# Optimization experiments

Measured on AMD Instinct MI355X. Metric: run time of the kernel, lower is better.

The kernel has to match this reference:

```python
import jax, jax.numpy as jnp
import numpy as np

B, S, D, H, L, V = 4, 512, 1024, 16, 4, 32000
DH = D // H
LATENT_START, N_LATENT, LATENT_ID = 64, 6, 5


def _ln(x, g, b):
    m = x.mean(-1, keepdims=True)
    v = ((x - m) ** 2).mean(-1, keepdims=True)
    return (x - m) * jax.lax.rsqrt(v + 1e-5) * g + b


def _model(x_emb, pos_ids, pos_emb, Wqkv, Wo, W1, W2, ln1_g, ln1_b, ln2_g, ln2_b, lnf_g, lnf_b, lm_head):
    # x_emb: [B,T,D]; returns (last_hidden [B,T,D] after final LN, logits [B,T,V])
    b, T, _ = x_emb.shape
    x = x_emb + pos_emb[pos_ids]
    causal = jnp.tril(jnp.ones((T, T), bool))
    for l in range(L):
        h = _ln(x, ln1_g[l], ln1_b[l])
        q, k, v = jnp.split(h @ Wqkv[l], 3, axis=-1)
        q = q.reshape(b, T, H, DH).transpose(0, 2, 1, 3)
        k = k.reshape(b, T, H, DH).transpose(0, 2, 1, 3)
        v = v.reshape(b, T, H, DH).transpose(0, 2, 1, 3)
        scores = jnp.einsum('bhqd,bhkd->bhqk', q, k) / np.float32(np.sqrt(DH))
        scores = jnp.where(causal, scores, jnp.float32(-1e9))
        attn = jax.nn.softmax(scores, axis=-1)
        o = jnp.einsum('bhqk,bhkd->bhqd', attn, v).transpose(0, 2, 1, 3).reshape(b, T, D)
        x = x + o @ Wo[l]
        h2 = _ln(x, ln2_g[l], ln2_b[l])
        x = x + jax.nn.gelu(h2 @ W1[l]) @ W2[l]
    hid = _ln(x, lnf_g, lnf_b)  # GPT2 hidden_states[-1] is post ln_f
    return hid, hid @ lm_head


def setup_inputs() -> dict:
    key = jax.random.key(0)
    ks = jax.random.split(key, 10)
    input_ids = jax.random.randint(ks[0], (B, S), 0, V, dtype=jnp.int32)
    input_ids = input_ids.at[:, LATENT_START:LATENT_START + N_LATENT].set(LATENT_ID)
    attention_mask = jnp.ones((B, S), jnp.int32)
    labels = jax.random.randint(ks[1], (B, S), 0, V, dtype=jnp.int32)
    position_ids = jnp.broadcast_to(jnp.arange(S, dtype=jnp.int32), (B, S))
    s = 0.02
    return {
        'input_ids': input_ids, 'attention_mask': attention_mask,
        'labels': labels, 'position_ids': position_ids,
        'emb': jax.random.normal(ks[2], (V, D), jnp.float32) * s,
        'pos_emb': jax.random.normal(ks[3], (S, D), jnp.float32) * s,
        'Wqkv': jax.random.normal(ks[4], (L, D, 3 * D), jnp.float32) * s,
        'Wo': jax.random.normal(ks[5], (L, D, D), jnp.float32) * s,
        'W1': jax.random.normal(ks[6], (L, D, 4 * D), jnp.float32) * s,
        'W2': jax.random.normal(ks[7], (L, 4 * D, D), jnp.float32) * s,
        'ln1_g': jnp.ones((L, D), jnp.float32), 'ln1_b': jnp.zeros((L, D), jnp.float32),
        'ln2_g': jnp.ones((L, D), jnp.float32), 'ln2_b': jnp.zeros((L, D), jnp.float32),
        'lnf_g': jnp.ones((D,), jnp.float32), 'lnf_b': jnp.zeros((D,), jnp.float32),
        'lm_head': jax.random.normal(ks[8], (D, V), jnp.float32) * s,
    }


def reference(input_ids, attention_mask, labels, position_ids, emb, pos_emb, Wqkv, Wo, W1, W2, ln1_g, ln1_b, ln2_g, ln2_b, lnf_g, lnf_b, lm_head):
    params = (pos_emb, Wqkv, Wo, W1, W2, ln1_g, ln1_b, ln2_g, ln2_b, lnf_g, lnf_b, lm_head)
    inputs_embeds = emb[input_ids]  # [B,S,D]
    start, end = 0, LATENT_START
    logits_list = []
    for p in range(N_LATENT):  # iterative latent passes
        hid, lg = _model(inputs_embeds[:, :end], position_ids[:, :end], *params)
        logits_list.append(lg[:, start:end])
        pos = LATENT_START + p
        # vectorized scatter: splice previous-position hidden state into latent slot
        inputs_embeds = inputs_embeds.at[:, pos, :].set(hid[:, pos - 1, :])
        start, end = end, (S if p + 1 >= N_LATENT else end + 1)
    hid, lg = _model(inputs_embeds[:, :end], position_ids[:, :end], *params)
    logits_list.append(lg[:, start:end])
    logits = jnp.concatenate(logits_list, axis=1)  # [B,S,V]
    shift_logits = logits[:, :-1]
    shift_labels = labels[:, 1:]
    logp = jax.nn.log_softmax(shift_logits, axis=-1)
    loss = -jnp.take_along_axis(logp, shift_labels[..., None], axis=-1).mean()
    return loss, inputs_embeds, logits
```

## Files before the change

kernel.cpp:

```cpp
#include <hip/hip_runtime.h>

static constexpr int BB  = 4;
static constexpr int SS  = 512;
static constexpr int DD  = 1024;
static constexpr int HH  = 16;
static constexpr int LL  = 4;
static constexpr int VV  = 32000;
static constexpr int DHH = 64;
static constexpr int FFF = 4096;

typedef short bf16x8  __attribute__((ext_vector_type(8)));
typedef short bf16x4v __attribute__((ext_vector_type(4)));
typedef float f32x4   __attribute__((ext_vector_type(4)));

__device__ __forceinline__ float b2f(ushort u){
  union { float f; unsigned int u32; } x; x.u32 = ((unsigned int)u) << 16; return x.f;
}
__device__ __forceinline__ ushort f2b(float f){
  union { float f; unsigned int u32; } x; x.f = f;
  unsigned int u = x.u32;
  return (ushort)((u + 0x7FFFu + ((u >> 16) & 1u)) >> 16);
}

__global__ __launch_bounds__(256) void convT_k(const float* __restrict__ in, ushort* __restrict__ out,
                                               int K, int N, long inStride, long outStride)
{
  in  += (long)blockIdx.z * inStride;
  out += (long)blockIdx.z * outStride;
  __shared__ float tile[64][65];
  int n0 = blockIdx.x * 64, k0 = blockIdx.y * 64;
  int tid = threadIdx.x;
  int cc = tid & 63, rr = tid >> 6;
#pragma unroll
  for (int i = 0; i < 16; i++){
    int r = rr + i * 4;
    tile[r][cc] = in[(long)(k0 + r) * N + n0 + cc];
  }
  __syncthreads();
#pragma unroll
  for (int i = 0; i < 16; i++){
    int r = rr + i * 4;
    out[(long)(n0 + r) * K + k0 + cc] = f2b(tile[cc][r]);
  }
}

__global__ __launch_bounds__(256) void embed_k(const int* __restrict__ ids, const float* __restrict__ emb,
                                               const float* __restrict__ pe, float* __restrict__ x,
                                               float* __restrict__ oemb)
{
  int t = blockIdx.x, b = blockIdx.y, tid = threadIdx.x;
  int id = ids[b * SS + t];
  float4 ev = *((const float4*)(emb + (long)id * DD) + tid);
  float4 pv = *((const float4*)(pe  + (long)t  * DD) + tid);
  *((float4*)(x + (long)(t * BB + b) * DD) + tid) =
      make_float4(ev.x + pv.x, ev.y + pv.y, ev.z + pv.z, ev.w + pv.w);
  float* op = oemb + ((long)b * SS + t) * DD + tid * 4;
  op[0] = ev.x; op[1] = ev.y; op[2] = ev.z; op[3] = ev.w;
}

__global__ __launch_bounds__(256) void ln_k(const float* __restrict__ xin, const float* __restrict__ g,
                                            const float* __restrict__ bt, ushort* __restrict__ out, long row0)
{
  long row = row0 + blockIdx.x;
  int tid = threadIdx.x;
  const float* rp = xin + row * DD;
  float4 v = *(const float4*)(rp + tid * 4);
  float s1 = v.x + v.y + v.z + v.w;
  float s2 = v.x * v.x + v.y * v.y + v.z * v.z + v.w * v.w;
#pragma unroll
  for (int o = 32; o; o >>= 1){ s1 += __shfl_down(s1, o); s2 += __shfl_down(s2, o); }
  __shared__ float red[2][4];
  int wv = tid >> 6, lane = tid & 63;
  if (lane == 0){ red[0][wv] = s1; red[1][wv] = s2; }
  __syncthreads();
  s1 = red[0][0] + red[0][1] + red[0][2] + red[0][3];
  s2 = red[1][0] + red[1][1] + red[1][2] + red[1][3];
  float mean = s1 * (1.0f / DD);
  float var  = s2 * (1.0f / DD) - mean * mean;
  float rstd = rsqrtf(var + 1e-5f);
  float4 gv = *(const float4*)(g + tid * 4);
  float4 bv = *(const float4*)(bt + tid * 4);
  ushort4 o4;
  o4.x = f2b((v.x - mean) * rstd * gv.x + bv.x);
  o4.y = f2b((v.y - mean) * rstd * gv.y + bv.y);
  o4.z = f2b((v.z - mean) * rstd * gv.z + bv.z);
  o4.w = f2b((v.w - mean) * rstd * gv.w + bv.w);
  *(ushort4*)(out + row * DD + tid * 4) = o4;
}

template<int EPI>
__device__ __forceinline__ void epi_store(float v, int grow, int ocol, void* Cv, int ldc,
                                          const float* Add, int t0, int l,
                                          ushort* kc, ushort* vc, ushort* qb)
{
  if constexpr (EPI == 1){
    float* Cf = (float*)Cv; long idx = (long)grow * ldc + ocol;
    Cf[idx] = v + Add[idx];
  } else if constexpr (EPI == 2){
    ushort* Cb = (ushort*)Cv; long idx = (long)grow * ldc + ocol;
    float tt = 0.7978845608028654f * (v + 0.044715f * v * v * v);
    Cb[idx] = f2b(0.5f * v * (1.0f + tanhf(tt)));
  } else if constexpr (EPI == 3){
    int t = t0 + (grow >> 2), b = grow & 3;
    ((float*)Cv)[((long)b * SS + t) * VV + ocol] = v;
  } else if constexpr (EPI == 4){
    if (ocol < DD){
      qb[((long)(t0 * BB + grow)) * DD + ocol] = f2b(v);
    } else {
      int t = t0 + (grow >> 2), b = grow & 3;
      int h = (ocol >> 6) & 15, d = ocol & 63;
      long dst = (((long)l * BB + b) * HH + h) * ((long)SS * DHH) + (long)t * DHH + d;
      if (ocol >= 2 * DD) vc[dst] = f2b(v); else kc[dst] = f2b(v);
    }
  }
}

template<int EPI>
__global__ __launch_bounds__(256) void gemm_k(const ushort* __restrict__ A, int lda,
                                              const ushort* __restrict__ BT,
                                              void* Cv, int ldc,
                                              const float* Add,
                                              int M, int N, int K, int gx,
                                              int l, int t0,
                                              ushort* kc, ushort* vc, ushort* qb,
                                              float* part, int KS)
{
  constexpr int BM  = 128;
  constexpr int MFR = 4;
  constexpr int NFR = 4;
  __shared__ ushort As[BM][72];
  __shared__ ushort Bs[128][72];
  int tid = threadIdx.x;
  int wv = tid >> 6, lane = tid & 63;
  int wm = wv >> 1, wn = wv & 1;

  int nwg = gridDim.x, orig = blockIdx.x;
  int wgid;
  if (nwg <= 1024){
    int qq = nwg >> 3, rr8 = nwg & 7, xcd = orig & 7;
    wgid = ((xcd < rr8) ? xcd * (qq + 1) : rr8 * (qq + 1) + (xcd - rr8) * qq) + (orig >> 3);
  } else {
    wgid = orig;
  }

  int gxy = gx * (N >> 7);
  int ksId = wgid / gxy;
  int rem  = wgid - ksId * gxy;
  int bx = rem % gx, by = rem / gx;
  int m0 = bx * BM, n0 = by * 128;
  int Kc = K / KS;
  int k_beg = ksId * Kc, k_end = k_beg + Kc;

  f32x4 acc[MFR][NFR];
  f32x4 zz = {0.f, 0.f, 0.f, 0.f};
#pragma unroll
  for (int m = 0; m < MFR; m++)
#pragma unroll
    for (int n = 0; n < NFR; n++) acc[m][n] = zz;

  int g4 = (lane >> 4) * 4;
  int rA = lane & 15;
  int arow = tid >> 3;
  int acol = (tid & 7) * 8;

  const ushort* Bp = BT + (long)(n0 + arow) * K + acol;
  long sB = 32 * (long)K;
  int gr0 = m0 + arow;       if (gr0 > M - 1) gr0 = M - 1;
  int gr1 = m0 + 32 + arow;  if (gr1 > M - 1) gr1 = M - 1;
  int gr2 = m0 + 64 + arow;  if (gr2 > M - 1) gr2 = M - 1;
  int gr3 = m0 + 96 + arow;  if (gr3 > M - 1) gr3 = M - 1;
  const ushort* Ap0 = A + (long)gr0 * lda + acol;
  const ushort* Ap1 = A + (long)gr1 * lda + acol;
  const ushort* Ap2 = A + (long)gr2 * lda + acol;
  const ushort* Ap3 = A + (long)gr3 * lda + acol;

  uint4 b0 = *(const uint4*)(Bp + k_beg);
  uint4 b1 = *(const uint4*)(Bp + sB + k_beg);
  uint4 b2 = *(const uint4*)(Bp + 2 * sB + k_beg);
  uint4 b3 = *(const uint4*)(Bp + 3 * sB + k_beg);
  uint4 a0 = *(const uint4*)(Ap0 + k_beg);
  uint4 a1 = *(const uint4*)(Ap1 + k_beg);
  uint4 a2 = *(const uint4*)(Ap2 + k_beg);
  uint4 a3 = *(const uint4*)(Ap3 + k_beg);

  for (int k0 = k_beg; k0 < k_end; k0 += 64){
    *(uint4*)&Bs[arow     ][acol] = b0;
    *(uint4*)&Bs[arow + 32][acol] = b1;
    *(uint4*)&Bs[arow + 64][acol] = b2;
    *(uint4*)&Bs[arow + 96][acol] = b3;
    *(uint4*)&As[arow     ][acol] = a0;
    *(uint4*)&As[arow + 32][acol] = a1;
    *(uint4*)&As[arow + 64][acol] = a2;
    *(uint4*)&As[arow + 96][acol] = a3;
    __syncthreads();
    int kn = k0 + 64;
    if (kn < k_end){
      b0 = *(const uint4*)(Bp + kn);
      b1 = *(const uint4*)(Bp + sB + kn);
      b2 = *(const uint4*)(Bp + 2 * sB + kn);
      b3 = *(const uint4*)(Bp + 3 * sB + kn);
      a0 = *(const uint4*)(Ap0 + kn);
      a1 = *(const uint4*)(Ap1 + kn);
      a2 = *(const uint4*)(Ap2 + kn);
      a3 = *(const uint4*)(Ap3 + kn);
    }
#pragma unroll
    for (int kk = 0; kk < 64; kk += 32){
      bf16x8 af[MFR], bfr[NFR];
#pragma unroll
      for (int m = 0; m < MFR; m++){
        int row = wm * 64 + m * 16 + rA;
        bf16x4v lo = *(const bf16x4v*)&As[row][kk + g4];
        bf16x4v hi = *(const bf16x4v*)&As[row][kk + 16 + g4];
        af[m] = __builtin_shufflevector(lo, hi, 0, 1, 2, 3, 4, 5, 6, 7);
      }
#pragma unroll
      for (int n = 0; n < NFR; n++){
        int row = wn * 64 + n * 16 + rA;
        bf16x4v lo = *(const bf16x4v*)&Bs[row][kk + g4];
        bf16x4v hi = *(const bf16x4v*)&Bs[row][kk + 16 + g4];
        bfr[n] = __builtin_shufflevector(lo, hi, 0, 1, 2, 3, 4, 5, 6, 7);
      }
#pragma unroll
      for (int m = 0; m < MFR; m++)
#pragma unroll
        for (int n = 0; n < NFR; n++)
          acc[m][n] = __builtin_amdgcn_mfma_f32_16x16x32_bf16(af[m], bfr[n], acc[m][n], 0, 0, 0);
    }
    __syncthreads();
  }

  int r4 = (lane >> 4) * 4;
#pragma unroll
  for (int m = 0; m < MFR; m++){
#pragma unroll
    for (int n = 0; n < NFR; n++){
      int orow = wm * 64 + m * 16 + r4;
      int ocol = n0 + wn * 64 + n * 16 + rA;
#pragma unroll
      for (int r = 0; r < 4; r++){
        int grow = m0 + orow + r;
        if (grow < M){
          if (KS > 1)
            part[(long)ksId * M * N + (long)grow * N + ocol] = acc[m][n][r];
          else
            epi_store<EPI>(acc[m][n][r], grow, ocol, Cv, ldc, Add, t0, l, kc, vc, qb);
        }
      }
    }
  }
}

template<int EPI>
__global__ __launch_bounds__(256) void sred_k(const float* __restrict__ part, int KS, int M, int N,
                                              void* Cv, int ldc, const float* Add,
                                              int l, int t0, ushort* kc, ushort* vc, ushort* qb)
{
  long i = (long)blockIdx.x * 256 + threadIdx.x;
  long MN = (long)M * N;
  if (i >= MN) return;
  float v = 0.f;
  for (int s = 0; s < KS; s++) v += part[s * MN + i];
  int m = (int)(i / N), n = (int)(i - (long)m * N);
  epi_store<EPI>(v, m, n, Cv, ldc, Add, t0, l, kc, vc, qb);
}

template<int TYPE>
__global__ __launch_bounds__(256) void dec_gemv_k(const float* xf, const ushort* ab,
                                                  const float* g, const float* bt,
                                                  const ushort* WT, float* x,
                                                  ushort* qb, ushort* kc, ushort* vc, ushort* gb,
                                                  int l, int pos)
{
  constexpr int K   = (TYPE == 3) ? FFF : DD;
  constexpr int NCH = K / 1024;
  int tid = threadIdx.x, wid = tid >> 6, lane = tid & 63;
  int n = blockIdx.x * 4 + wid;

  float acc[4] = {0.f, 0.f, 0.f, 0.f};

#pragma unroll
  for (int ch = 0; ch < NCH; ch++){
    int ks = ch * 1024 + lane * 16;
    float a[4][16];
    if constexpr (TYPE == 0 || TYPE == 2){
#pragma unroll
      for (int r = 0; r < 4; r++){
        const float* rp = xf + (long)(pos * BB + r) * DD + ks;
#pragma unroll
        for (int q = 0; q < 4; q++){
          float4 v = *(const float4*)(rp + q * 4);
          a[r][q*4+0] = v.x; a[r][q*4+1] = v.y; a[r][q*4+2] = v.z; a[r][q*4+3] = v.w;
        }
      }
      float gj[16], bj[16];
#pragma unroll
      for (int q = 0; q < 4; q++){
        float4 gv = *(const float4*)(g  + ks + q * 4);
        float4 bv = *(const float4*)(bt + ks + q * 4);
        gj[q*4+0]=gv.x; gj[q*4+1]=gv.y; gj[q*4+2]=gv.z; gj[q*4+3]=gv.w;
        bj[q*4+0]=bv.x; bj[q*4+1]=bv.y; bj[q*4+2]=bv.z; bj[q*4+3]=bv.w;
      }
#pragma unroll
      for (int r = 0; r < 4; r++){
        float s1 = 0.f, s2 = 0.f;
#pragma unroll
        for (int j = 0; j < 16; j++){ s1 += a[r][j]; s2 += a[r][j] * a[r][j]; }
#pragma unroll
        for (int o = 32; o; o >>= 1){ s1 += __shfl_xor(s1, o); s2 += __shfl_xor(s2, o); }
        float mean = s1 * (1.0f / DD);
        float var  = s2 * (1.0f / DD) - mean * mean;
        float rstd = rsqrtf(var + 1e-5f);
#pragma unroll
        for (int j = 0; j < 16; j++)
          a[r][j] = b2f(f2b((a[r][j] - mean) * rstd * gj[j] + bj[j]));
      }
    } else {
      constexpr int AD = (TYPE == 3) ? FFF : DD;
#pragma unroll
      for (int r = 0; r < 4; r++){
        const ushort* rp = ab + (long)(pos * BB + r) * AD + ks;
        uint4 pa = *(const uint4*)rp;
        uint4 pb = *(const uint4*)(rp + 8);
        const unsigned int w[8] = {pa.x, pa.y, pa.z, pa.w, pb.x, pb.y, pb.z, pb.w};
#pragma unroll
        for (int q = 0; q < 8; q++){
          a[r][q*2]   = b2f((ushort)(w[q] & 0xffff));
          a[r][q*2+1] = b2f((ushort)(w[q] >> 16));
        }
      }
    }
    {
      const ushort* wp = WT + (long)n * K + ks;
      uint4 pa = *(const uint4*)wp;
      uint4 pb = *(const uint4*)(wp + 8);
      const unsigned int w[8] = {pa.x, pa.y, pa.z, pa.w, pb.x, pb.y, pb.z, pb.w};
      float wf[16];
#pragma unroll
      for (int q = 0; q < 8; q++){
        wf[q*2]   = b2f((ushort)(w[q] & 0xffff));
        wf[q*2+1] = b2f((ushort)(w[q] >> 16));
      }
#pragma unroll
      for (int r = 0; r < 4; r++){
        float s = 0.f;
#pragma unroll
        for (int j = 0; j < 16; j++) s += a[r][j] * wf[j];
        acc[r] += s;
      }
    }
  }

#pragma unroll
  for (int r = 0; r < 4; r++)
#pragma unroll
    for (int o = 32; o; o >>= 1) acc[r] += __shfl_xor(acc[r], o);

  if (lane < 4){
    int r = lane;
    long Rrow = (long)(pos * BB + r);
    float v = acc[r];
    if constexpr (TYPE == 0){
      if (n < DD){
        qb[Rrow * DD + n] = f2b(v);
      } else if (n < 2 * DD){
        int h = (n - DD) >> 6, d = n & 63;
        kc[(((long)l * BB + r) * HH + h) * ((long)SS * DHH) + (long)pos * DHH + d] = f2b(v);
      } else {
        int h = (n - 2 * DD) >> 6, d = n & 63;
        vc[(((long)l * BB + r) * HH + h) * ((long)SS * DHH) + (long)pos * DHH + d] = f2b(v);
      }
    } else if constexpr (TYPE == 2){
      float tt = 0.7978845608028654f * (v + 0.044715f * v * v * v);
      gb[Rrow * FFF + n] = f2b(0.5f * v * (1.0f + tanhf(tt)));
    } else {
      long idx = Rrow * DD + n;
      x[idx] = x[idx] + v;
    }
  }
}

__global__ __launch_bounds__(256) void dec_final_k(const float* xf, const float* g, const float* bt,
                                                   const float* pe, ushort* hid, float* x,
                                                   float* oemb, int pos)
{
  int wid = threadIdx.x >> 6, lane = threadIdx.x & 63;
  long R = (long)(pos * BB + wid);
  const float* rp = xf + R * DD + lane * 16;
  float a[16];
#pragma unroll
  for (int q = 0; q < 4; q++){
    float4 v = *(const float4*)(rp + q * 4);
    a[q*4+0] = v.x; a[q*4+1] = v.y; a[q*4+2] = v.z; a[q*4+3] = v.w;
  }
  float s1 = 0.f, s2 = 0.f;
#pragma unroll
  for (int j = 0; j < 16; j++){ s1 += a[j]; s2 += a[j] * a[j]; }
#pragma unroll
  for (int o = 32; o; o >>= 1){ s1 += __shfl_xor(s1, o); s2 += __shfl_xor(s2, o); }
  float mean = s1 * (1.0f / DD);
  float var  = s2 * (1.0f / DD) - mean * mean;
  float rstd = rsqrtf(var + 1e-5f);
  int pn = pos + 1;
#pragma unroll
  for (int j = 0; j < 16; j++){
    int d = lane * 16 + j;
    ushort hb = f2b((a[j] - mean) * rstd * g[d] + bt[d]);
    hid[R * DD + d] = hb;
    float hv = b2f(hb);
    oemb[((long)wid * SS + pn) * DD + d] = hv;
    x[((long)(pn * BB + wid)) * DD + d] = hv + pe[(long)pn * DD + d];
  }
}

__global__ __launch_bounds__(256) void attn_k(const ushort* __restrict__ qb, const ushort* __restrict__ kc,
                                              const ushort* __restrict__ vc, ushort* __restrict__ o,
                                              int l, int t0, int Tc)
{
  __shared__ float sc[4][512];
  __shared__ float qs[4][64];
  int tid = threadIdx.x, wv = tid >> 6, lane = tid & 63;
  int b = blockIdx.z, h = blockIdx.y;
  int qrow = blockIdx.x * 4 + wv;
  bool act = qrow < Tc;
  int tq = t0 + qrow;
  long kvoff = (((long)l * BB + b) * HH + h) * ((long)SS * DHH);
  const ushort* kb = kc + kvoff;
  const ushort* vb = vc + kvoff;
  if (act) qs[wv][lane] = b2f(qb[((long)(tq * BB + b)) * DD + h * DHH + lane]);
  __syncthreads();
  int nk = act ? (tq + 1) : 0;
  float m = -3.0e38f;
  for (int key = lane; key < nk; key += 64){
    const ushort* kp = kb + (long)key * DHH;
    float s = 0.f;
#pragma unroll
    for (int j = 0; j < 8; j++){
      uint4 kvv = *(const uint4*)(kp + j * 8);
      s += qs[wv][j*8+0] * b2f((ushort)(kvv.x & 0xffff));
      s += qs[wv][j*8+1] * b2f((ushort)(kvv.x >> 16));
      s += qs[wv][j*8+2] * b2f((ushort)(kvv.y & 0xffff));
      s += qs[wv][j*8+3] * b2f((ushort)(kvv.y >> 16));
      s += qs[wv][j*8+4] * b2f((ushort)(kvv.z & 0xffff));
      s += qs[wv][j*8+5] * b2f((ushort)(kvv.z >> 16));
      s += qs[wv][j*8+6] * b2f((ushort)(kvv.w & 0xffff));
      s += qs[wv][j*8+7] * b2f((ushort)(kvv.w >> 16));
    }
    s *= 0.125f;
    sc[wv][key] = s;
    m = fmaxf(m, s);
  }
#pragma unroll
  for (int off = 32; off; off >>= 1) m = fmaxf(m, __shfl_xor(m, off));
  float ssum = 0.f;
  for (int key = lane; key < nk; key += 64){
    float p = expf(sc[wv][key] - m);
    sc[wv][key] = p;
    ssum += p;
  }
#pragma unroll
  for (int off = 32; off; off >>= 1) ssum += __shfl_xor(ssum, off);
  __syncthreads();
  float accv = 0.f;
  int key = 0;
  for (; key + 3 < nk; key += 4){
    float p0 = sc[wv][key],     p1 = sc[wv][key + 1];
    float p2 = sc[wv][key + 2], p3 = sc[wv][key + 3];
    float v0 = b2f(vb[(long)key * DHH + lane]);
    float v1 = b2f(vb[(long)(key + 1) * DHH + lane]);
    float v2 = b2f(vb[(long)(key + 2) * DHH + lane]);
    float v3 = b2f(vb[(long)(key + 3) * DHH + lane]);
    accv += p0 * v0 + p1 * v1 + p2 * v2 + p3 * v3;
  }
  for (; key < nk; key++)
    accv += sc[wv][key] * b2f(vb[(long)key * DHH + lane]);
  if (act) o[((long)(tq * BB + b)) * DD + h * DHH + lane] = f2b(accv / ssum);
}

__global__ __launch_bounds__(256) void advance_k(const ushort* __restrict__ hid, const float* __restrict__ pe,
                                                 float* __restrict__ x, float* __restrict__ oemb, int pos)
{
  int d = blockIdx.x * 256 + threadIdx.x;
  int b = blockIdx.y;
  float hv = b2f(hid[((long)((pos - 1) * BB + b)) * DD + d]);
  oemb[((long)b * SS + pos) * DD + d] = hv;
  x[((long)(pos * BB + b)) * DD + d] = hv + pe[(long)pos * DD + d];
}

__global__ __launch_bounds__(256) void loss_rows_k(const float* __restrict__ logits, const int* __restrict__ labels,
                                                   float* __restrict__ rowloss)
{
  int t = blockIdx.x, b = blockIdx.y, tid = threadIdx.x;
  const float* row = logits + ((long)b * SS + t) * VV;
  float m = -3.0e38f, s = 0.f;
  auto upd = [&](float v){
    if (v > m){ s = s * expf(m - v) + 1.f; m = v; }
    else s += expf(v - m);
  };
  if (tid < 3) upd(row[tid]);
  if (tid == 3) upd(row[VV - 1]);
  const float4* vrow = (const float4*)(row + 3);
  for (int i = tid; i < 7999; i += 256){
    float4 v = vrow[i];
    upd(v.x); upd(v.y); upd(v.z); upd(v.w);
  }
#pragma unroll
  for (int off = 32; off; off >>= 1){
    float om = __shfl_xor(m, off), os = __shfl_xor(s, off);
    float nm = fmaxf(m, om);
    s = s * expf(m - nm) + os * expf(om - nm);
    m = nm;
  }
  __shared__ float sm[4], ssb[4];
  if ((tid & 63) == 0){ sm[tid >> 6] = m; ssb[tid >> 6] = s; }
  __syncthreads();
  if (tid == 0){
    float M = fmaxf(fmaxf(sm[0], sm[1]), fmaxf(sm[2], sm[3]));
    float S = ssb[0] * expf(sm[0] - M) + ssb[1] * expf(sm[1] - M)
            + ssb[2] * expf(sm[2] - M) + ssb[3] * expf(sm[3] - M);
    int lab = labels[b * SS + t + 1];
    rowloss[b * (SS - 1) + t] = (M + logf(S)) - row[lab];
  }
}

__global__ __launch_bounds__(256) void loss_final_k(const float* __restrict__ rowloss, float* __restrict__ out)
{
  int tid = threadIdx.x;
  float s = 0.f;
  for (int i = tid; i < BB * (SS - 1); i += 256) s += rowloss[i];
#pragma unroll
  for (int o = 32; o; o >>= 1) s += __shfl_down(s, o);
  __shared__ float red[4];
  if ((tid & 63) == 0) red[tid >> 6] = s;
  __syncthreads();
  if (tid == 0) out[0] = (red[0] + red[1] + red[2] + red[3]) / (float)(BB * (SS - 1));
}

static inline int cdiv_i(int a, int b){ return (a + b - 1) / b; }

extern "C" void kernel_launch(void* const* d_in, const int* in_sizes, int n_in,
                              void* d_out, int out_size, void* d_ws, size_t ws_size,
                              hipStream_t stream)
{
  (void)in_sizes; (void)n_in; (void)out_size; (void)ws_size;
  const int*   ids    = (const int*)d_in[0];
  const int*   labels = (const int*)d_in[2];
  const float* emb    = (const float*)d_in[4];
  const float* pe     = (const float*)d_in[5];
  const float* Wqkv   = (const float*)d_in[6];
  const float* Wo     = (const float*)d_in[7];
  const float* W1     = (const float*)d_in[8];
  const float* W2     = (const float*)d_in[9];
  const float* ln1g   = (const float*)d_in[10];
  const float* ln1b   = (const float*)d_in[11];
  const float* ln2g   = (const float*)d_in[12];
  const float* ln2b   = (const float*)d_in[13];
  const float* lnfg   = (const float*)d_in[14];
  const float* lnfb   = (const float*)d_in[15];
  const float* lm     = (const float*)d_in[16];

  float* out_loss   = (float*)d_out;
  float* out_emb    = out_loss + 1;
  float* out_logits = out_emb + (size_t)BB * SS * DD;

  char* wsp = (char*)d_ws;
  size_t off = 0;
  auto alloc = [&](size_t bytes) -> void* {
    void* p = wsp + off; off += (bytes + 255) & ~(size_t)255; return p;
  };
  ushort* wqkvT = (ushort*)alloc((size_t)LL * 3 * DD * DD * 2);
  ushort* woT   = (ushort*)alloc((size_t)LL * DD * DD * 2);
  ushort* w1T   = (ushort*)alloc((size_t)LL * FFF * DD * 2);
  ushort* w2T   = (ushort*)alloc((size_t)LL * DD * FFF * 2);
  ushort* lmT   = (ushort*)alloc((size_t)VV * DD * 2);
  float*  x     = (float*)alloc((size_t)BB * SS * DD * 4);
  ushort* hbuf  = (ushort*)alloc((size_t)BB * SS * DD * 2);
  ushort* qbuf  = (ushort*)alloc((size_t)BB * SS * DD * 2);
  ushort* obuf  = (ushort*)alloc((size_t)BB * SS * DD * 2);
  ushort* gbuf  = (ushort*)alloc((size_t)BB * SS * FFF * 2);
  ushort* hid   = (ushort*)alloc((size_t)BB * SS * DD * 2);
  ushort* kcache= (ushort*)alloc((size_t)LL * BB * SS * DD * 2);
  ushort* vcache= (ushort*)alloc((size_t)LL * BB * SS * DD * 2);
  float*  rowls = (float*)alloc((size_t)BB * (SS - 1) * 4);
  float*  part  = out_logits;

  convT_k<<<dim3(3 * DD / 64, DD / 64, LL), dim3(256), 0, stream>>>(Wqkv, wqkvT, DD, 3 * DD, (long)DD * 3 * DD, (long)3 * DD * DD);
  convT_k<<<dim3(DD / 64, DD / 64, LL),     dim3(256), 0, stream>>>(Wo,   woT,  DD, DD,     (long)DD * DD,     (long)DD * DD);
  convT_k<<<dim3(FFF / 64, DD / 64, LL),    dim3(256), 0, stream>>>(W1,   w1T,  DD, FFF,    (long)DD * FFF,    (long)FFF * DD);
  convT_k<<<dim3(DD / 64, FFF / 64, LL),    dim3(256), 0, stream>>>(W2,   w2T,  FFF, DD,    (long)FFF * DD,    (long)DD * FFF);
  convT_k<<<dim3(VV / 64, DD / 64, 1),      dim3(256), 0, stream>>>(lm,   lmT,  DD, VV,     0, 0);

  embed_k<<<dim3(SS, BB), dim3(256), 0, stream>>>(ids, emb, pe, x, out_emb);

  const int ct0[7] = {0, 64, 65, 66, 67, 68, 69};
  const int ct1[7] = {64, 65, 66, 67, 68, 69, 512};

  auto g128 = [&](int epi, const ushort* A, int lda, const ushort* BT, void* C, int ldc,
                  const float* Add, int M, int N, int K, int l, int t0, int KS){
    int gx = cdiv_i(M, 128);
    int nwg = gx * (N >> 7) * KS;
    if (epi == 1) gemm_k<1><<<nwg, 256, 0, stream>>>(A, lda, BT, C, ldc, Add, M, N, K, gx, l, t0, kcache, vcache, qbuf, part, KS);
    if (epi == 2) gemm_k<2><<<nwg, 256, 0, stream>>>(A, lda, BT, C, ldc, Add, M, N, K, gx, l, t0, kcache, vcache, qbuf, part, KS);
    if (epi == 3) gemm_k<3><<<nwg, 256, 0, stream>>>(A, lda, BT, C, ldc, Add, M, N, K, gx, l, t0, kcache, vcache, qbuf, part, KS);
    if (epi == 4) gemm_k<4><<<nwg, 256, 0, stream>>>(A, lda, BT, C, ldc, Add, M, N, K, gx, l, t0, kcache, vcache, qbuf, part, KS);
    if (KS > 1){
      int nred = cdiv_i(M * N, 256);
      if (epi == 1) sred_k<1><<<nred, 256, 0, stream>>>(part, KS, M, N, C, ldc, Add, l, t0, kcache, vcache, qbuf);
      if (epi == 2) sred_k<2><<<nred, 256, 0, stream>>>(part, KS, M, N, C, ldc, Add, l, t0, kcache, vcache, qbuf);
      if (epi == 4) sred_k<4><<<nred, 256, 0, stream>>>(part, KS, M, N, C, ldc, Add, l, t0, kcache, vcache, qbuf);
    }
  };

  for (int c = 0; c < 7; c++){
    int t0 = ct0[c];
    int Tc = ct1[c] - t0;
    int M  = Tc * BB;
    long roff = (long)t0 * BB;

    if (Tc == 1){
      int pos = t0;
      for (int l = 0; l < LL; l++){
        dec_gemv_k<0><<<dim3(3 * DD / 4), dim3(256), 0, stream>>>(x, nullptr, ln1g + l * DD, ln1b + l * DD,
            wqkvT + (long)l * 3 * DD * DD, nullptr, qbuf, kcache, vcache, nullptr, l, pos);
        attn_k<<<dim3(1, HH, BB), dim3(64), 0, stream>>>(qbuf, kcache, vcache, obuf, l, t0, Tc);
        dec_gemv_k<1><<<dim3(DD / 4), dim3(256), 0, stream>>>(nullptr, obuf, nullptr, nullptr,
            woT + (long)l * DD * DD, x, nullptr, nullptr, nullptr, nullptr, l, pos);
        dec_gemv_k<2><<<dim3(FFF / 4), dim3(256), 0, stream>>>(x, nullptr, ln2g + l * DD, ln2b + l * DD,
            w1T + (long)l * FFF * DD, nullptr, nullptr, nullptr, nullptr, gbuf, l, pos);
        dec_gemv_k<3><<<dim3(DD / 4), dim3(256), 0, stream>>>(nullptr, gbuf, nullptr, nullptr,
            w2T + (long)l * DD * FFF, x, nullptr, nullptr, nullptr, nullptr, l, pos);
      }
      dec_final_k<<<dim3(1), dim3(256), 0, stream>>>(x, lnfg, lnfb, pe, hid, x, out_emb, pos);
    } else {
      bool small = (M <= 256);
      int ksQKV = small ? 4 : 2;
      int ksWO  = small ? 8 : 2;
      int ksW1  = small ? 4 : 2;
      int ksW2  = small ? 8 : 2;
      for (int l = 0; l < LL; l++){
        ln_k<<<dim3(M), dim3(256), 0, stream>>>(x, ln1g + l * DD, ln1b + l * DD, hbuf, roff);
        g128(4, hbuf + roff * DD, DD, wqkvT + (long)l * 3 * DD * DD, nullptr, 0, nullptr, M, 3 * DD, DD, l, t0, ksQKV);
        attn_k<<<dim3(cdiv_i(Tc, 4), HH, BB), dim3(256), 0, stream>>>(qbuf, kcache, vcache, obuf, l, t0, Tc);
        g128(1, obuf + roff * DD, DD, woT + (long)l * DD * DD, x + roff * DD, DD, x + roff * DD, M, DD, DD, l, t0, ksWO);
        ln_k<<<dim3(M), dim3(256), 0, stream>>>(x, ln2g + l * DD, ln2b + l * DD, hbuf, roff);
        g128(2, hbuf + roff * DD, DD, w1T + (long)l * FFF * DD, gbuf + roff * FFF, FFF, nullptr, M, FFF, DD, l, t0, ksW1);
        g128(1, gbuf + roff * FFF, FFF, w2T + (long)l * DD * FFF, x + roff * DD, DD, x + roff * DD, M, DD, FFF, l, t0, ksW2);
      }
      ln_k<<<dim3(M), dim3(256), 0, stream>>>(x, lnfg, lnfb, hid, roff);
      if (c == 0)
        advance_k<<<dim3(DD / 256, BB), dim3(256), 0, stream>>>(hid, pe, x, out_emb, 64);
    }
  }

  g128(3, hid, DD, lmT, out_logits, 0, nullptr, BB * SS, VV, DD, 0, 0, 1);

  loss_rows_k<<<dim3(SS - 1, BB), dim3(256), 0, stream>>>(out_logits, labels, rowls);
  loss_final_k<<<dim3(1), dim3(256), 0, stream>>>(rowls, out_loss);
}
```

Measured before the change: 2.934 ms.

## Add 128x256-tile GEMM for LM head and drop split-K for large QKV/W1

Adds a new 512-thread MFMA GEMM kernel with 128x256 tiles and register-prefetched global loads, used for the large LM-head projection in place of the generic 128-tile GEMM. Its epilogue writes logits directly in [B,S,V] order. Separately, split-K is turned off for the QKV and W1 GEMMs when M is large, which removes the partial-sum buffer round trip and the reduction kernel. The larger tile uses more LDS and registers, so occupancy may drop, and the single-split GEMMs launch fewer workgroups.

```diff
diff --git a/kernel.cpp b/kernel.cpp
--- a/kernel.cpp
+++ b/kernel.cpp
@@ -251,6 +251,111 @@
   }
 }
 
+__global__ __launch_bounds__(512) void gemm256_k(const ushort* __restrict__ A, int lda,
+                                                 const ushort* __restrict__ BT,
+                                                 float* __restrict__ Cv,
+                                                 int M, int N, int K, int gx, int t0)
+{
+  constexpr int MFR = 4;
+  constexpr int NFR = 4;
+  __shared__ ushort As[128][72];
+  __shared__ ushort Bs[256][72];
+  int tid = threadIdx.x;
+  int wv = tid >> 6, lane = tid & 63;
+  int wm = wv >> 2, wn = wv & 3;
+
+  int wgid = blockIdx.x;
+  int bx = wgid % gx, by = wgid / gx;
+  int m0 = bx * 128, n0 = by * 256;
+
+  f32x4 acc[MFR][NFR];
+  f32x4 zz = {0.f, 0.f, 0.f, 0.f};
+#pragma unroll
+  for (int m = 0; m < MFR; m++)
+#pragma unroll
+    for (int n = 0; n < NFR; n++) acc[m][n] = zz;
+
+  int g4 = (lane >> 4) * 4;
+  int rA = lane & 15;
+  int srow = tid >> 3;
+  int scol = (tid & 7) * 8;
+
+  long sB = 64 * (long)K;
+  const ushort* Bp = BT + (long)(n0 + srow) * K + scol;
+  int ga0 = m0 + srow;       if (ga0 > M - 1) ga0 = M - 1;
+  int ga1 = m0 + 64 + srow;  if (ga1 > M - 1) ga1 = M - 1;
+  const ushort* Ap0 = A + (long)ga0 * lda + scol;
+  const ushort* Ap1 = A + (long)ga1 * lda + scol;
+
+  uint4 b0 = *(const uint4*)(Bp);
+  uint4 b1 = *(const uint4*)(Bp + sB);
+  uint4 b2 = *(const uint4*)(Bp + 2 * sB);
+  uint4 b3 = *(const uint4*)(Bp + 3 * sB);
+  uint4 a0 = *(const uint4*)(Ap0);
+  uint4 a1 = *(const uint4*)(Ap1);
+
+  for (int k0 = 0; k0 < K; k0 += 64){
+    *(uint4*)&Bs[srow      ][scol] = b0;
+    *(uint4*)&Bs[srow + 64 ][scol] = b1;
+    *(uint4*)&Bs[srow + 128][scol] = b2;
+    *(uint4*)&Bs[srow + 192][scol] = b3;
+    *(uint4*)&As[srow      ][scol] = a0;
+    *(uint4*)&As[srow + 64 ][scol] = a1;
+    __syncthreads();
+    int kn = k0 + 64;
+    if (kn < K){
+      b0 = *(const uint4*)(Bp + kn);
+      b1 = *(const uint4*)(Bp + sB + kn);
+      b2 = *(const uint4*)(Bp + 2 * sB + kn);
+      b3 = *(const uint4*)(Bp + 3 * sB + kn);
+      a0 = *(const uint4*)(Ap0 + kn);
+      a1 = *(const uint4*)(Ap1 + kn);
+    }
+#pragma unroll
+    for (int kk = 0; kk < 64; kk += 32){
+      bf16x8 af[MFR], bfr[NFR];
+#pragma unroll
+      for (int m = 0; m < MFR; m++){
+        int row = wm * 64 + m * 16 + rA;
+        bf16x4v lo = *(const bf16x4v*)&As[row][kk + g4];
+        bf16x4v hi = *(const bf16x4v*)&As[row][kk + 16 + g4];
+        af[m] = __builtin_shufflevector(lo, hi, 0, 1, 2, 3, 4, 5, 6, 7);
+      }
+#pragma unroll
+      for (int n = 0; n < NFR; n++){
+        int row = wn * 64 + n * 16 + rA;
+        bf16x4v lo = *(const bf16x4v*)&Bs[row][kk + g4];
+        bf16x4v hi = *(const bf16x4v*)&Bs[row][kk + 16 + g4];
+        bfr[n] = __builtin_shufflevector(lo, hi, 0, 1, 2, 3, 4, 5, 6, 7);
+      }
+#pragma unroll
+      for (int m = 0; m < MFR; m++)
+#pragma unroll
+        for (int n = 0; n < NFR; n++)
+          acc[m][n] = __builtin_amdgcn_mfma_f32_16x16x32_bf16(af[m], bfr[n], acc[m][n], 0, 0, 0);
+    }
+    __syncthreads();
+  }
+
+  int r4 = (lane >> 4) * 4;
+#pragma unroll
+  for (int m = 0; m < MFR; m++){
+#pragma unroll
+    for (int n = 0; n < NFR; n++){
+      int orow = wm * 64 + m * 16 + r4;
+      int ocol = n0 + wn * 64 + n * 16 + rA;
+#pragma unroll
+      for (int r = 0; r < 4; r++){
+        int grow = m0 + orow + r;
+        if (grow < M){
+          int t = t0 + (grow >> 2), b = grow & 3;
+          Cv[((long)b * SS + t) * VV + ocol] = acc[m][n][r];
+        }
+      }
+    }
+  }
+}
+
 template<int EPI>
 __global__ __launch_bounds__(256) void sred_k(const float* __restrict__ part, int KS, int M, int N,
                                               void* Cv, int ldc, const float* Add,
@@ -633,9 +738,9 @@
       dec_final_k<<<dim3(1), dim3(256), 0, stream>>>(x, lnfg, lnfb, pe, hid, x, out_emb, pos);
     } else {
       bool small = (M <= 256);
-      int ksQKV = small ? 4 : 2;
+      int ksQKV = small ? 4 : 1;
       int ksWO  = small ? 8 : 2;
-      int ksW1  = small ? 4 : 2;
+      int ksW1  = small ? 4 : 1;
       int ksW2  = small ? 8 : 2;
       for (int l = 0; l < LL; l++){
         ln_k<<<dim3(M), dim3(256), 0, stream>>>(x, ln1g + l * DD, ln1b + l * DD, hbuf, roff);
@@ -652,7 +757,11 @@
     }
   }
 
-  g128(3, hid, DD, lmT, out_logits, 0, nullptr, BB * SS, VV, DD, 0, 0, 1);
+  {
+    int gx = BB * SS / 128;
+    int nwg = gx * (VV / 256);
+    gemm256_k<<<nwg, 512, 0, stream>>>(hid, DD, lmT, out_logits, BB * SS, VV, DD, gx, 0);
+  }
 
   loss_rows_k<<<dim3(SS - 1, BB), dim3(256), 0, stream>>>(out_logits, labels, rowls);
   loss_final_k<<<dim3(1), dim3(256), 0, stream>>>(rowls, out_loss);
```

Result: no change. 2.879 ms (-1.9%).

## Fuse decode steps into a persistent cooperative kernel with grid syncs

Applied to the files above, without the earlier changes.

Replaces the roughly 105 small per-layer decode kernel launches for the five single-token latent steps with one persistent cooperative kernel. It uses grid-wide syncs between the QKV, attention, Wo, W1 and W2 phases and the final LN. It also moves the split-K partial buffer into its own workspace allocation instead of aliasing the logits, and lowers split-K for the large chunk's QKV and W1 GEMMs from 2 to 1. The aim is to remove launch overhead and tail idle time; the cost is 25 grid barriers per step on only 256 blocks, which may underuse bandwidth for the weight streaming.

```diff
diff --git a/kernel.cpp b/kernel.cpp
--- a/kernel.cpp
+++ b/kernel.cpp
@@ -1,4 +1,5 @@
 #include <hip/hip_runtime.h>
+#include <hip/hip_cooperative_groups.h>
 
 static constexpr int BB  = 4;
 static constexpr int SS  = 512;
@@ -413,6 +414,248 @@
   }
 }
 
+struct DecParams {
+  const float* pe;
+  float* x;
+  ushort* qb; ushort* kc; ushort* vc; ushort* gb; ushort* ob;
+  ushort* hid; float* oemb;
+  const ushort* wqkvT; const ushort* woT; const ushort* w1T; const ushort* w2T;
+  const float* ln1g; const float* ln1b; const float* ln2g; const float* ln2b;
+  const float* lnfg; const float* lnfb;
+};
+
+template<int TYPE>
+__device__ __forceinline__ void dec_gemv_ln_phase(const DecParams& p, int l, int pos,
+                                                  int gw, int nw, int lane)
+{
+  constexpr int NCOLS = (TYPE == 0) ? 3 * DD : FFF;
+  const ushort* WT = (TYPE == 0) ? p.wqkvT + (long)l * 3 * DD * DD
+                                 : p.w1T   + (long)l * FFF * DD;
+  const float* g  = ((TYPE == 0) ? p.ln1g : p.ln2g) + l * DD;
+  const float* bt = ((TYPE == 0) ? p.ln1b : p.ln2b) + l * DD;
+  int ks = lane * 16;
+  float a[4][16];
+#pragma unroll
+  for (int r = 0; r < 4; r++){
+    const float* rp = p.x + (long)(pos * BB + r) * DD + ks;
+#pragma unroll
+    for (int q = 0; q < 4; q++){
+      float4 v = *(const float4*)(rp + q * 4);
+      a[r][q*4+0] = v.x; a[r][q*4+1] = v.y; a[r][q*4+2] = v.z; a[r][q*4+3] = v.w;
+    }
+  }
+  float gj[16], bj[16];
+#pragma unroll
+  for (int q = 0; q < 4; q++){
+    float4 gv = *(const float4*)(g  + ks + q * 4);
+    float4 bv = *(const float4*)(bt + ks + q * 4);
+    gj[q*4+0]=gv.x; gj[q*4+1]=gv.y; gj[q*4+2]=gv.z; gj[q*4+3]=gv.w;
+    bj[q*4+0]=bv.x; bj[q*4+1]=bv.y; bj[q*4+2]=bv.z; bj[q*4+3]=bv.w;
+  }
+#pragma unroll
+  for (int r = 0; r < 4; r++){
+    float s1 = 0.f, s2 = 0.f;
+#pragma unroll
+    for (int j = 0; j < 16; j++){ s1 += a[r][j]; s2 += a[r][j] * a[r][j]; }
+#pragma unroll
+    for (int o = 32; o; o >>= 1){ s1 += __shfl_xor(s1, o); s2 += __shfl_xor(s2, o); }
+    float mean = s1 * (1.0f / DD);
+    float var  = s2 * (1.0f / DD) - mean * mean;
+    float rstd = rsqrtf(var + 1e-5f);
+#pragma unroll
+    for (int j = 0; j < 16; j++)
+      a[r][j] = b2f(f2b((a[r][j] - mean) * rstd * gj[j] + bj[j]));
+  }
+  for (int n = gw; n < NCOLS; n += nw){
+    const ushort* wp = WT + (long)n * DD + ks;
+    uint4 pa = *(const uint4*)wp;
+    uint4 pb = *(const uint4*)(wp + 8);
+    const unsigned int w[8] = {pa.x, pa.y, pa.z, pa.w, pb.x, pb.y, pb.z, pb.w};
+    float wf[16];
+#pragma unroll
+    for (int q = 0; q < 8; q++){
+      wf[q*2]   = b2f((ushort)(w[q] & 0xffff));
+      wf[q*2+1] = b2f((ushort)(w[q] >> 16));
+    }
+    float acc[4];
+#pragma unroll
+    for (int r = 0; r < 4; r++){
+      float s = 0.f;
+#pragma unroll
+      for (int j = 0; j < 16; j++) s += a[r][j] * wf[j];
+      acc[r] = s;
+    }
+#pragma unroll
+    for (int r = 0; r < 4; r++)
+#pragma unroll
+      for (int o = 32; o; o >>= 1) acc[r] += __shfl_xor(acc[r], o);
+    if (lane < 4){
+      int r = lane;
+      long Rrow = (long)(pos * BB + r);
+      float v = acc[r];
+      if constexpr (TYPE == 0){
+        if (n < DD){
+          p.qb[Rrow * DD + n] = f2b(v);
+        } else if (n < 2 * DD){
+          int h = (n - DD) >> 6, d = n & 63;
+          p.kc[(((long)l * BB + r) * HH + h) * ((long)SS * DHH) + (long)pos * DHH + d] = f2b(v);
+        } else {
+          int h = (n - 2 * DD) >> 6, d = n & 63;
+          p.vc[(((long)l * BB + r) * HH + h) * ((long)SS * DHH) + (long)pos * DHH + d] = f2b(v);
+        }
+      } else {
+        float tt = 0.7978845608028654f * (v + 0.044715f * v * v * v);
+        p.gb[Rrow * FFF + n] = f2b(0.5f * v * (1.0f + tanhf(tt)));
+      }
+    }
+  }
+}
+
+template<int TYPE>
+__device__ __forceinline__ void dec_gemv_res_phase(const DecParams& p, int l, int pos,
+                                                   int gw, int nw, int lane)
+{
+  constexpr int K   = (TYPE == 3) ? FFF : DD;
+  constexpr int NCH = K / 1024;
+  const ushort* WT = (TYPE == 1) ? p.woT + (long)l * DD * DD : p.w2T + (long)l * DD * FFF;
+  const ushort* ab = (TYPE == 1) ? p.ob : p.gb;
+  for (int n = gw; n < DD; n += nw){
+    float acc[4] = {0.f, 0.f, 0.f, 0.f};
+#pragma unroll
+    for (int ch = 0; ch < NCH; ch++){
+      int ks = ch * 1024 + lane * 16;
+      const ushort* wp = WT + (long)n * K + ks;
+      uint4 wa = *(const uint4*)wp;
+      uint4 wb = *(const uint4*)(wp + 8);
+      const unsigned int w[8] = {wa.x, wa.y, wa.z, wa.w, wb.x, wb.y, wb.z, wb.w};
+      float wf[16];
+#pragma unroll
+      for (int q = 0; q < 8; q++){
+        wf[q*2]   = b2f((ushort)(w[q] & 0xffff));
+        wf[q*2+1] = b2f((ushort)(w[q] >> 16));
+      }
+#pragma unroll
+      for (int r = 0; r < 4; r++){
+        const ushort* rp = ab + (long)(pos * BB + r) * K + ks;
+        uint4 xa = *(const uint4*)rp;
+        uint4 xb = *(const uint4*)(rp + 8);
+        const unsigned int xw[8] = {xa.x, xa.y, xa.z, xa.w, xb.x, xb.y, xb.z, xb.w};
+        float s = 0.f;
+#pragma unroll
+        for (int q = 0; q < 8; q++){
+          s += b2f((ushort)(xw[q] & 0xffff)) * wf[q*2];
+          s += b2f((ushort)(xw[q] >> 16))    * wf[q*2+1];
+        }
+        acc[r] += s;
+      }
+    }
+#pragma unroll
+    for (int r = 0; r < 4; r++)
+#pragma unroll
+      for (int o = 32; o; o >>= 1) acc[r] += __shfl_xor(acc[r], o);
+    if (lane < 4){
+      long idx = (long)(pos * BB + lane) * DD + n;
+      p.x[idx] = p.x[idx] + acc[lane];
+    }
+  }
+}
+
+__global__ __launch_bounds__(256) void dec_all_k(DecParams p)
+{
+  cooperative_groups::grid_group grid = cooperative_groups::this_grid();
+  int tid = threadIdx.x, wid = tid >> 6, lane = tid & 63;
+  int gw = blockIdx.x * 4 + wid;
+  int nw = gridDim.x * 4;
+  __shared__ float qs[4][64];
+  __shared__ float ps[4][80];
+
+  for (int step = 0; step < 5; step++){
+    int pos = 64 + step;
+    for (int l = 0; l < LL; l++){
+      dec_gemv_ln_phase<0>(p, l, pos, gw, nw, lane);
+      __threadfence(); grid.sync(); __threadfence();
+      if (gw < BB * HH){
+        int b = gw >> 4, h = gw & 15;
+        long kvoff = (((long)l * BB + b) * HH + h) * ((long)SS * DHH);
+        const ushort* kb = p.kc + kvoff;
+        const ushort* vb = p.vc + kvoff;
+        qs[wid][lane] = b2f(p.qb[((long)(pos * BB + b)) * DD + h * DHH + lane]);
+        int nk = pos + 1;
+        float m = -3.0e38f;
+        for (int key = lane; key < nk; key += 64){
+          const ushort* kp = kb + (long)key * DHH;
+          float s = 0.f;
+#pragma unroll
+          for (int j = 0; j < 8; j++){
+            uint4 kvv = *(const uint4*)(kp + j * 8);
+            s += qs[wid][j*8+0] * b2f((ushort)(kvv.x & 0xffff));
+            s += qs[wid][j*8+1] * b2f((ushort)(kvv.x >> 16));
+            s += qs[wid][j*8+2] * b2f((ushort)(kvv.y & 0xffff));
+            s += qs[wid][j*8+3] * b2f((ushort)(kvv.y >> 16));
+            s += qs[wid][j*8+4] * b2f((ushort)(kvv.z & 0xffff));
+            s += qs[wid][j*8+5] * b2f((ushort)(kvv.z >> 16));
+            s += qs[wid][j*8+6] * b2f((ushort)(kvv.w & 0xffff));
+            s += qs[wid][j*8+7] * b2f((ushort)(kvv.w >> 16));
+          }
+          s *= 0.125f;
+          ps[wid][key] = s;
+          m = fmaxf(m, s);
+        }
+#pragma unroll
+        for (int off = 32; off; off >>= 1) m = fmaxf(m, __shfl_xor(m, off));
+        float ssum = 0.f;
+        for (int key = lane; key < nk; key += 64){
+          float pv = expf(ps[wid][key] - m);
+          ps[wid][key] = pv;
+          ssum += pv;
+        }
+#pragma unroll
+        for (int off = 32; off; off >>= 1) ssum += __shfl_xor(ssum, off);
+        float accv = 0.f;
+        for (int key = 0; key < nk; key++)
+          accv += ps[wid][key] * b2f(vb[(long)key * DHH + lane]);
+        p.ob[((long)(pos * BB + b)) * DD + h * DHH + lane] = f2b(accv / ssum);
+      }
+      __threadfence(); grid.sync(); __threadfence();
+      dec_gemv_res_phase<1>(p, l, pos, gw, nw, lane);
+      __threadfence(); grid.sync(); __threadfence();
+      dec_gemv_ln_phase<2>(p, l, pos, gw, nw, lane);
+      __threadfence(); grid.sync(); __threadfence();
+      dec_gemv_res_phase<3>(p, l, pos, gw, nw, lane);
+      __threadfence(); grid.sync(); __threadfence();
+    }
+    if (blockIdx.x == 0){
+      long R = (long)(pos * BB + wid);
+      const float* rp = p.x + R * DD + lane * 16;
+      float a[16];
+#pragma unroll
+      for (int q = 0; q < 4; q++){
+        float4 v = *(const float4*)(rp + q * 4);
+        a[q*4+0] = v.x; a[q*4+1] = v.y; a[q*4+2] = v.z; a[q*4+3] = v.w;
+      }
+      float s1 = 0.f, s2 = 0.f;
+#pragma unroll
+      for (int j = 0; j < 16; j++){ s1 += a[j]; s2 += a[j] * a[j]; }
+#pragma unroll
+      for (int o = 32; o; o >>= 1){ s1 += __shfl_xor(s1, o); s2 += __shfl_xor(s2, o); }
+      float mean = s1 * (1.0f / DD);
+      float var  = s2 * (1.0f / DD) - mean * mean;
+      float rstd = rsqrtf(var + 1e-5f);
+      int pn = pos + 1;
+#pragma unroll
+      for (int j = 0; j < 16; j++){
+        int d = lane * 16 + j;
+        ushort hb = f2b((a[j] - mean) * rstd * p.lnfg[d] + p.lnfb[d]);
+        p.hid[R * DD + d] = hb;
+        float hv = b2f(hb);
+        p.oemb[((long)wid * SS + pn) * DD + d] = hv;
+        p.x[((long)(pn * BB + wid)) * DD + d] = hv + p.pe[(long)pn * DD + d];
+      }
+    }
+    __threadfence(); grid.sync(); __threadfence();
+  }
+}
+
 __global__ __launch_bounds__(256) void attn_k(const ushort* __restrict__ qb, const ushort* __restrict__ kc,
                                               const ushort* __restrict__ vc, ushort* __restrict__ o,
                                               int l, int t0, int Tc)
@@ -581,8 +824,8 @@
   ushort* hid   = (ushort*)alloc((size_t)BB * SS * DD * 2);
   ushort* kcache= (ushort*)alloc((size_t)LL * BB * SS * DD * 2);
   ushort* vcache= (ushort*)alloc((size_t)LL * BB * SS * DD * 2);
+  float*  part  = (float*)alloc((size_t)17 * 1024 * 1024);
   float*  rowls = (float*)alloc((size_t)BB * (SS - 1) * 4);
-  float*  part  = out_logits;
 
   convT_k<<<dim3(3 * DD / 64, DD / 64, LL), dim3(256), 0, stream>>>(Wqkv, wqkvT, DD, 3 * DD, (long)DD * 3 * DD, (long)3 * DD * DD);
   convT_k<<<dim3(DD / 64, DD / 64, LL),     dim3(256), 0, stream>>>(Wo,   woT,  DD, DD,     (long)DD * DD,     (long)DD * DD);
@@ -591,9 +834,6 @@
   convT_k<<<dim3(VV / 64, DD / 64, 1),      dim3(256), 0, stream>>>(lm,   lmT,  DD, VV,     0, 0);
 
   embed_k<<<dim3(SS, BB), dim3(256), 0, stream>>>(ids, emb, pe, x, out_emb);
-
-  const int ct0[7] = {0, 64, 65, 66, 67, 68, 69};
-  const int ct1[7] = {64, 65, 66, 67, 68, 69, 512};
 
   auto g128 = [&](int epi, const ushort* A, int lda, const ushort* BT, void* C, int ldc,
                   const float* Add, int M, int N, int K, int l, int t0, int KS){
@@ -611,18 +851,45 @@
     }
   };
 
-  for (int c = 0; c < 7; c++){
-    int t0 = ct0[c];
-    int Tc = ct1[c] - t0;
-    int M  = Tc * BB;
+  auto big_chunk = [&](int t0, int Tc){
+    int M = Tc * BB;
     long roff = (long)t0 * BB;
-
-    if (Tc == 1){
-      int pos = t0;
+    bool small = (M <= 256);
+    int ksQKV = small ? 4 : 1;
+    int ksWO  = small ? 8 : 2;
+    int ksW1  = small ? 4 : 1;
+    int ksW2  = small ? 8 : 2;
+    for (int l = 0; l < LL; l++){
+      ln_k<<<dim3(M), dim3(256), 0, stream>>>(x, ln1g + l * DD, ln1b + l * DD, hbuf, roff);
+      g128(4, hbuf + roff * DD, DD, wqkvT + (long)l * 3 * DD * DD, nullptr, 0, nullptr, M, 3 * DD, DD, l, t0, ksQKV);
+      attn_k<<<dim3(cdiv_i(Tc, 4), HH, BB), dim3(256), 0, stream>>>(qbuf, kcache, vcache, obuf, l, t0, Tc);
+      g128(1, obuf + roff * DD, DD, woT + (long)l * DD * DD, x + roff * DD, DD, x + roff * DD, M, DD, DD, l, t0, ksWO);
+      ln_k<<<dim3(M), dim3(256), 0, stream>>>(x, ln2g + l * DD, ln2b + l * DD, hbuf, roff);
+      g128(2, hbuf + roff * DD, DD, w1T + (long)l * FFF * DD, gbuf + roff * FFF, FFF, nullptr, M, FFF, DD, l, t0, ksW1);
+      g128(1, gbuf + roff * FFF, FFF, w2T + (long)l * DD * FFF, x + roff * DD, DD, x + roff * DD, M, DD, FFF, l, t0, ksW2);
+    }
+    ln_k<<<dim3(M), dim3(256), 0, stream>>>(x, lnfg, lnfb, hid, roff);
+  };
+
+  big_chunk(0, 64);
+  advance_k<<<dim3(DD / 256, BB), dim3(256), 0, stream>>>(hid, pe, x, out_emb, 64);
+
+  DecParams dp;
+  dp.pe = pe; dp.x = x; dp.qb = qbuf; dp.kc = kcache; dp.vc = vcache; dp.gb = gbuf;
+  dp.ob = obuf; dp.hid = hid; dp.oemb = out_emb;
+  dp.wqkvT = wqkvT; dp.woT = woT; dp.w1T = w1T; dp.w2T = w2T;
+  dp.ln1g = ln1g; dp.ln1b = ln1b; dp.ln2g = ln2g; dp.ln2b = ln2b;
+  dp.lnfg = lnfg; dp.lnfb = lnfb;
+  void* dargs[] = { (void*)&dp };
+  hipError_t coopErr = hipLaunchCooperativeKernel((const void*)dec_all_k, dim3(256), dim3(256),
+                                                  dargs, 0, stream);
+  if (coopErr != hipSuccess){
+    for (int step = 0; step < 5; step++){
+      int pos = 64 + step;
       for (int l = 0; l < LL; l++){
         dec_gemv_k<0><<<dim3(3 * DD / 4), dim3(256), 0, stream>>>(x, nullptr, ln1g + l * DD, ln1b + l * DD,
             wqkvT + (long)l * 3 * DD * DD, nullptr, qbuf, kcache, vcache, nullptr, l, pos);
-        attn_k<<<dim3(1, HH, BB), dim3(64), 0, stream>>>(qbuf, kcache, vcache, obuf, l, t0, Tc);
+        attn_k<<<dim3(1, HH, BB), dim3(64), 0, stream>>>(qbuf, kcache, vcache, obuf, l, pos, 1);
         dec_gemv_k<1><<<dim3(DD / 4), dim3(256), 0, stream>>>(nullptr, obuf, nullptr, nullptr,
             woT + (long)l * DD * DD, x, nullptr, nullptr, nullptr, nullptr, l, pos);
         dec_gemv_k<2><<<dim3(FFF / 4), dim3(256), 0, stream>>>(x, nullptr, ln2g + l * DD, ln2b + l * DD,
@@ -631,26 +898,10 @@
             w2T + (long)l * DD * FFF, x, nullptr, nullptr, nullptr, nullptr, l, pos);
       }
       dec_final_k<<<dim3(1), dim3(256), 0, stream>>>(x, lnfg, lnfb, pe, hid, x, out_emb, pos);
-    } else {
-      bool small = (M <= 256);
-      int ksQKV = small ? 4 : 2;
-      int ksWO  = small ? 8 : 2;
-      int ksW1  = small ? 4 : 2;
-      int ksW2  = small ? 8 : 2;
-      for (int l = 0; l < LL; l++){
-        ln_k<<<dim3(M), dim3(256), 0, stream>>>(x, ln1g + l * DD, ln1b + l * DD, hbuf, roff);
-        g128(4, hbuf + roff * DD, DD, wqkvT + (long)l * 3 * DD * DD, nullptr, 0, nullptr, M, 3 * DD, DD, l, t0, ksQKV);
-        attn_k<<<dim3(cdiv_i(Tc, 4), HH, BB), dim3(256), 0, stream>>>(qbuf, kcache, vcache, obuf, l, t0, Tc);
-        g128(1, obuf + roff * DD, DD, woT + (long)l * DD * DD, x + roff * DD, DD, x + roff * DD, M, DD, DD, l, t0, ksWO);
-        ln_k<<<dim3(M), dim3(256), 0, stream>>>(x, ln2g + l * DD, ln2b + l * DD, hbuf, roff);
-        g128(2, hbuf + roff * DD, DD, w1T + (long)l * FFF * DD, gbuf + roff * FFF, FFF, nullptr, M, FFF, DD, l, t0, ksW1);
-        g128(1, gbuf + roff * FFF, FFF, w2T + (long)l * DD * FFF, x + roff * DD, DD, x + roff * DD, M, DD, FFF, l, t0, ksW2);
-      }
-      ln_k<<<dim3(M), dim3(256), 0, stream>>>(x, lnfg, lnfb, hid, roff);
-      if (c == 0)
-        advance_k<<<dim3(DD / 256, BB), dim3(256), 0, stream>>>(hid, pe, x, out_emb, 64);
-    }
-  }
+    }
+  }
+
+  big_chunk(69, 512 - 69);
 
   g128(3, hid, DD, lmT, out_logits, 0, nullptr, BB * SS, VV, DD, 0, 0, 1);
 
```

Measured after the change: 9.525 ms. +224.6%, slower.
